# Performance work log

Hardware: AMD Instinct MI355X
Metric: run time of the kernel (lower is better)

## Reference

```python
import jax, jax.numpy as jnp
import numpy as np

PI = 3.1415  # the module hard-codes 3.1415, not math.pi


def setup_inputs() -> dict:
    nt, ns, nh, ng = 1000, 1024, 64, 32
    key = jax.random.key(0)
    kP, kE, kT1, kT2, kxc, kW, kb = jax.random.split(key, 7)
    # physically plausible forcings: P, E >= 0; T2 > T1 always
    P = jax.random.uniform(kP, (nt, ns)) * 10.0
    E = jax.random.uniform(kE, (nt, ns)) * 5.0
    T1 = jax.random.normal(kT1, (nt, ns)) * 10.0
    T2 = T1 + jax.random.uniform(kT2, (nt, ns)) * 10.0 + 0.1
    x = jnp.stack([P, E, T1, T2], axis=-1)  # [nt, ns, 4]
    xc = jax.random.normal(kxc, (ns, ng))
    std = 1.0 / np.sqrt(nh)  # reset_parameters: uniform(-std, std)
    W3 = jax.random.uniform(kW, (nh * 4, ng), minval=-std, maxval=std)
    b3 = jax.random.uniform(kb, (nh * 4,), minval=-std, maxval=std)
    return {"x": x, "xc": xc, "W3": W3, "b3": b3}


def reference(x, xc, W3, b3):
    nh = W3.shape[0] // 4
    P, E, T1, T2 = x[..., 0], x[..., 1], x[..., 2], x[..., 3]  # each [nt, ns]
    Ta = (T1 + T2) * 0.5
    melted = T1 >= 0.0
    frozen = T2 <= 0.0
    masked = melted | frozen
    # NaN-safe arccos: out-of-range args occur exactly where masked overrides apply
    arg = jnp.where(masked, 0.0, jnp.clip((T1 + T2) / (T2 - T1), -1.0, 1.0))
    rP = 1.0 - jnp.arccos(arg) / PI
    rP = jnp.where(melted, 1.0, jnp.where(frozen, 0.0, rP))
    Ps = (1.0 - rP) * P  # snow fraction
    Pl = rP * P          # liquid fraction
    # static gates (fc3 on catchment attributes); dropout is identity in eval
    w = xc @ W3.T + b3  # [ns, 4*nh]
    gm = jnp.exp(w[:, :nh]) + 1.0
    ge = jax.nn.sigmoid(w[:, nh:2 * nh])
    go = jax.nn.sigmoid(w[:, 2 * nh:3 * nh])
    ga = jax.nn.softmax(w[:, 3 * nh:], axis=1)

    ns = P.shape[1]
    S0 = jnp.zeros((ns, nh), dtype=x.dtype)
    H0 = jnp.zeros((ns, nh), dtype=x.dtype)

    def step(carry, inp):
        S0, H0 = carry
        Ps_k, Pl_k, E_k, Ta_k = inp  # each [ns]
        Sm = jnp.minimum(S0, jax.nn.relu(Ta_k[:, None] * gm))  # snowmelt
        S = S0 + Ps_k[:, None]
        H = jax.nn.relu(H0 + Sm + Pl_k[:, None] - E_k[:, None] * ge)
        Q = H * go
        Y = jnp.sum(Q * ga, axis=1)  # [ns]
        return (S - Sm, H - Q), Y

    _, Yout = jax.lax.scan(step, (S0, H0), (Ps, Pl, E, Ta))
    return Yout  # [nt, ns]
```

## Files before the change

kernel.cpp:

```cpp
#include <hip/hip_runtime.h>
#include <math.h>

#define NH 64
#define NG 32
#define LROW 68

__global__ __launch_bounds__(64) void waternet_kernel(
    const float* __restrict__ x,
    const float* __restrict__ xc,
    const float* __restrict__ W3,
    const float* __restrict__ b3,
    float* __restrict__ out,
    int nt, int ns)
{
    const int b    = blockIdx.x;
    const int s    = (b & 7) * (ns >> 3) + (b >> 3);
    const int lane = threadIdx.x;

    __shared__ float yb[2][NH * LROW];
    __shared__ float scal[NH * 4];

    float wq[4];
    #pragma unroll
    for (int q = 0; q < 4; ++q) {
        const float4* row = reinterpret_cast<const float4*>(W3 + (size_t)(q * NH + lane) * NG);
        const float4* xr  = reinterpret_cast<const float4*>(xc + (size_t)s * NG);
        float a = 0.f;
        #pragma unroll
        for (int g = 0; g < NG / 4; ++g) {
            const float4 w  = row[g];
            const float4 xv = xr[g];
            a = fmaf(w.x, xv.x, a); a = fmaf(w.y, xv.y, a);
            a = fmaf(w.z, xv.z, a); a = fmaf(w.w, xv.w, a);
        }
        wq[q] = a + b3[q * NH + lane];
    }
    const float gm = expf(wq[0]) + 1.0f;
    const float ge = 1.0f / (1.0f + expf(-wq[1]));
    const float go = 1.0f / (1.0f + expf(-wq[2]));
    float mx = wq[3];
    #pragma unroll
    for (int o = 32; o; o >>= 1) mx = fmaxf(mx, __shfl_xor(mx, o, 64));
    const float ex = expf(wq[3] - mx);
    float smx = ex;
    #pragma unroll
    for (int o = 32; o; o >>= 1) smx += __shfl_xor(smx, o, 64);
    const float ga = ex / smx;
    const float gq = go * ga;
    const float gk = 1.0f - go;

    float S = 0.f, H = 0.f;
    const int nfull = nt / NH;
    const int tail  = nt - nfull * NH;

    int tp = min(lane, nt - 1);
    float4 f = *reinterpret_cast<const float4*>(x + ((size_t)tp * ns + s) * 4);

    #define PHASE_A() { \
        const float P = f.x, E = f.y, T1 = f.z, T2 = f.w; \
        const float Ta  = 0.5f * (T1 + T2); \
        const float arg = fminf(1.f, fmaxf(-1.f, (T1 + T2) / (T2 - T1))); \
        const float aa  = fabsf(arg); \
        float p = fmaf(aa, -0.0012624911f, 0.0066700901f); \
        p = fmaf(aa, p, -0.0170881256f); p = fmaf(aa, p, 0.0308918810f); \
        p = fmaf(aa, p, -0.0501743046f); p = fmaf(aa, p, 0.0889789874f); \
        p = fmaf(aa, p, -0.2145988016f); p = fmaf(aa, p, 1.5707963050f); \
        const float rr0 = sqrtf(1.f - aa) * p;                   \
        const float ac  = (arg >= 0.f) ? rr0 : (3.14159265358979f - rr0); \
        const float rr  = 1.f - ac * (1.0f / 3.1415f);           \
        const float rP  = (T1 >= 0.f) ? 1.f : ((T2 <= 0.f) ? 0.f : rr); \
        float4 st; st.x = fmaxf(Ta, 0.f); st.y = (1.f - rP) * P; \
        st.z = rP * P;  st.w = E; \
        *reinterpret_cast<float4*>(&scal[lane * 4]) = st; \
    }

    #define STEP_BODY(sc, YB, J) { \
        const float M   = sc.x * gm;                      \
        const float Sm  = fminf(S, M);                    \
        const float tmp = fmaf(-sc.w, ge, sc.z);          \
        const float Hn  = fmaxf(H + Sm + tmp, 0.f); \
        S = (S + sc.y) - Sm; \
        H = Hn * gk; \
        (YB)[(J) * LROW + lane] = Hn * gq; \
    }

    for (int c = 0; c < nfull; ++c) {
        PHASE_A();

        tp = min((c + 1) * NH + lane, nt - 1);
        const float4 fn = *reinterpret_cast<const float4*>(x + ((size_t)tp * ns + s) * 4);

        float*       ybw = yb[c & 1];
        const float* ybr = yb[(c & 1) ^ 1];
        float z0 = 0.f, z1 = 0.f, z2 = 0.f, z3 = 0.f;

        #pragma unroll
        for (int j = 0; j < NH; ++j) {
            const float4 sc = *reinterpret_cast<const float4*>(&scal[j * 4]);
            STEP_BODY(sc, ybw, j)
            if ((j & 3) == 1) {
                const float4 v = *reinterpret_cast<const float4*>(&ybr[lane * LROW + (j >> 2) * 4]);
                z0 += v.x; z1 += v.y; z2 += v.z; z3 += v.w;
            }
        }
        if (c > 0)
            out[(size_t)((c - 1) * NH + lane) * ns + s] = (z0 + z1) + (z2 + z3);
        f = fn;
    }

    if (nfull > 0) {
        const float* row = &yb[(nfull - 1) & 1][lane * LROW];
        float z0 = 0.f, z1 = 0.f, z2 = 0.f, z3 = 0.f;
        #pragma unroll
        for (int g = 0; g < NH / 4; ++g) {
            const float4 v = *reinterpret_cast<const float4*>(&row[g * 4]);
            z0 += v.x; z1 += v.y; z2 += v.z; z3 += v.w;
        }
        out[(size_t)((nfull - 1) * NH + lane) * ns + s] = (z0 + z1) + (z2 + z3);
    }

    if (tail > 0) {
        PHASE_A();
        float* ybw = yb[nfull & 1];
        for (int j = 0; j < tail; ++j) {
            const float4 sc = *reinterpret_cast<const float4*>(&scal[j * 4]);
            STEP_BODY(sc, ybw, j)
        }
        if (lane < tail) {
            const float* row = &ybw[lane * LROW];
            float z0 = 0.f, z1 = 0.f, z2 = 0.f, z3 = 0.f;
            #pragma unroll
            for (int g = 0; g < NH / 4; ++g) {
                const float4 v = *reinterpret_cast<const float4*>(&row[g * 4]);
                z0 += v.x; z1 += v.y; z2 += v.z; z3 += v.w;
            }
            out[(size_t)(nfull * NH + lane) * ns + s] = (z0 + z1) + (z2 + z3);
        }
    }
    #undef PHASE_A
    #undef STEP_BODY
}

extern "C" void kernel_launch(void* const* d_in, const int* in_sizes, int n_in,
                              void* d_out, int out_size, void* d_ws, size_t ws_size,
                              hipStream_t stream) {
    const float* x  = (const float*)d_in[0];
    const float* xc = (const float*)d_in[1];
    const float* W3 = (const float*)d_in[2];
    const float* b3 = (const float*)d_in[3];
    float* out = (float*)d_out;

    const int nh = in_sizes[3] / 4;
    const int ng = in_sizes[2] / (4 * nh);
    const int ns = in_sizes[1] / ng;
    const int nt = in_sizes[0] / (ns * 4);

    waternet_kernel<<<dim3(ns), dim3(64), 0, stream>>>(x, xc, W3, b3, out, nt, ns);
}
```

Before: 111.6 us.

## Batch recurrence steps by eight and drop double-buffered reduction overlap

Restructures the per-chunk time loop into batches of eight steps that load the scalar forcings and precompute the independent melt thresholds and net inputs before the serial chain runs. The snow-melt min is rewritten as S - max(S-M, 0), which makes S = max(S-M,0) + Ps and shortens the dependent chain. The double-buffered output tile, which overlapped the previous chunk's reduction with the current recurrence, is replaced by a single tile reduced right after each chunk. This uses less shared memory but removes the reduction overlap, and the outer loop is kept from unrolling.

```diff
diff --git a/kernel.cpp b/kernel.cpp
--- a/kernel.cpp
+++ b/kernel.cpp
@@ -3,7 +3,7 @@
 
 #define NH 64
 #define NG 32
-#define LROW 68
+#define YROW 68
 
 __global__ __launch_bounds__(64) void waternet_kernel(
     const float* __restrict__ x,
@@ -17,7 +17,7 @@
     const int s    = (b & 7) * (ns >> 3) + (b >> 3);
     const int lane = threadIdx.x;
 
-    __shared__ float yb[2][NH * LROW];
+    __shared__ float ytile[NH * YROW];
     __shared__ float scal[NH * 4];
 
     float wq[4];
@@ -74,60 +74,66 @@
         *reinterpret_cast<float4*>(&scal[lane * 4]) = st; \
     }
 
-    #define STEP_BODY(sc, YB, J) { \
-        const float M   = sc.x * gm;                      \
-        const float Sm  = fminf(S, M);                    \
-        const float tmp = fmaf(-sc.w, ge, sc.z);          \
-        const float Hn  = fmaxf(H + Sm + tmp, 0.f); \
-        S = (S + sc.y) - Sm; \
-        H = Hn * gk; \
-        (YB)[(J) * LROW + lane] = Hn * gq; \
+    #define BATCH8(j0) { \
+        float4 sc[8]; float M[8], w[8]; \
+        _Pragma("unroll") \
+        for (int k = 0; k < 8; ++k) \
+            sc[k] = *reinterpret_cast<const float4*>(&scal[((j0) + k) * 4]);  \
+        _Pragma("unroll") \
+        for (int k = 0; k < 8; ++k) { M[k] = sc[k].x * gm; w[k] = fmaf(-sc[k].w, ge, sc[k].z); } \
+        _Pragma("unroll") \
+        for (int k = 0; k < 8; ++k) { \
+            const float u  = S - M[k]; \
+            const float um = fmaxf(u, 0.f);         \
+            const float Sm = S - um;                \
+            S = um + sc[k].y;                       \
+            const float a  = Sm + w[k]; \
+            const float Hn = fmaxf(H + a, 0.f); \
+            H = Hn * gk; \
+            ytile[((j0) + k) * YROW + lane] = Hn * gq; \
+        } \
     }
 
+    #pragma unroll 1
     for (int c = 0; c < nfull; ++c) {
         PHASE_A();
 
         tp = min((c + 1) * NH + lane, nt - 1);
         const float4 fn = *reinterpret_cast<const float4*>(x + ((size_t)tp * ns + s) * 4);
 
-        float*       ybw = yb[c & 1];
-        const float* ybr = yb[(c & 1) ^ 1];
-        float z0 = 0.f, z1 = 0.f, z2 = 0.f, z3 = 0.f;
+        #pragma unroll
+        for (int bb = 0; bb < NH / 8; ++bb) BATCH8(bb * 8)
 
-        #pragma unroll
-        for (int j = 0; j < NH; ++j) {
-            const float4 sc = *reinterpret_cast<const float4*>(&scal[j * 4]);
-            STEP_BODY(sc, ybw, j)
-            if ((j & 3) == 1) {
-                const float4 v = *reinterpret_cast<const float4*>(&ybr[lane * LROW + (j >> 2) * 4]);
+        {
+            const float* row = &ytile[lane * YROW];
+            float z0 = 0.f, z1 = 0.f, z2 = 0.f, z3 = 0.f;
+            #pragma unroll
+            for (int g = 0; g < NH / 4; ++g) {
+                const float4 v = *reinterpret_cast<const float4*>(&row[g * 4]);
                 z0 += v.x; z1 += v.y; z2 += v.z; z3 += v.w;
             }
+            out[(size_t)(c * NH + lane) * ns + s] = (z0 + z1) + (z2 + z3);
         }
-        if (c > 0)
-            out[(size_t)((c - 1) * NH + lane) * ns + s] = (z0 + z1) + (z2 + z3);
         f = fn;
-    }
-
-    if (nfull > 0) {
-        const float* row = &yb[(nfull - 1) & 1][lane * LROW];
-        float z0 = 0.f, z1 = 0.f, z2 = 0.f, z3 = 0.f;
-        #pragma unroll
-        for (int g = 0; g < NH / 4; ++g) {
-            const float4 v = *reinterpret_cast<const float4*>(&row[g * 4]);
-            z0 += v.x; z1 += v.y; z2 += v.z; z3 += v.w;
-        }
-        out[(size_t)((nfull - 1) * NH + lane) * ns + s] = (z0 + z1) + (z2 + z3);
     }
 
     if (tail > 0) {
         PHASE_A();
-        float* ybw = yb[nfull & 1];
-        for (int j = 0; j < tail; ++j) {
+        const int nb = tail / 8;
+        for (int bb = 0; bb < nb; ++bb) BATCH8(bb * 8)
+        for (int j = nb * 8; j < tail; ++j) {
             const float4 sc = *reinterpret_cast<const float4*>(&scal[j * 4]);
-            STEP_BODY(sc, ybw, j)
+            const float M  = sc.x * gm;
+            const float w  = fmaf(-sc.w, ge, sc.z);
+            const float um = fmaxf(S - M, 0.f);
+            const float Sm = S - um;
+            S = um + sc.y;
+            const float Hn = fmaxf(H + Sm + w, 0.f);
+            H = Hn * gk;
+            ytile[j * YROW + lane] = Hn * gq;
         }
         if (lane < tail) {
-            const float* row = &ybw[lane * LROW];
+            const float* row = &ytile[lane * YROW];
             float z0 = 0.f, z1 = 0.f, z2 = 0.f, z3 = 0.f;
             #pragma unroll
             for (int g = 0; g < NH / 4; ++g) {
@@ -138,7 +144,7 @@
         }
     }
     #undef PHASE_A
-    #undef STEP_BODY
+    #undef BATCH8
 }
 
 extern "C" void kernel_launch(void* const* d_in, const int* in_sizes, int n_in,
```

New measurement: 109.2 us. 2.1% less time.

## Split recurrence and forcing/reduction work across two warp-specialized wavefronts

Applied to the files above, without the earlier changes.

Blocks grow to two wavefronts. The first runs only the serial S/H recurrence, storing raw H per step. The second loads and preprocesses the next chunk's forcings and does the gq-weighted reduction of the previous chunk's H tile into the output. The intent is to take forcing loads, the arccos work and the output reduction off the critical recurrence path, and to lighten its step by folding the gq multiply into the reducer. In exchange it adds a __syncthreads per chunk, double-buffered scal, and more shared memory and threads per block.

```diff
diff --git a/kernel.cpp b/kernel.cpp
--- a/kernel.cpp
+++ b/kernel.cpp
@@ -3,9 +3,9 @@
 
 #define NH 64
 #define NG 32
-#define LROW 68
+#define YROW 68
 
-__global__ __launch_bounds__(64) void waternet_kernel(
+__global__ __launch_bounds__(128) void waternet_kernel(
     const float* __restrict__ x,
     const float* __restrict__ xc,
     const float* __restrict__ W3,
@@ -15,10 +15,13 @@
 {
     const int b    = blockIdx.x;
     const int s    = (b & 7) * (ns >> 3) + (b >> 3);
-    const int lane = threadIdx.x;
+    const int tid  = threadIdx.x;
+    const int lane = tid & 63;
+    const bool crit = (tid < 64);
 
-    __shared__ float yb[2][NH * LROW];
-    __shared__ float scal[NH * 4];
+    __shared__ float ytile[2][NH * YROW];
+    __shared__ float scal[2][NH * 4];
+    __shared__ float gqbuf[NH];
 
     float wq[4];
     #pragma unroll
@@ -49,15 +52,12 @@
     const float gq = go * ga;
     const float gk = 1.0f - go;
 
-    float S = 0.f, H = 0.f;
-    const int nfull = nt / NH;
-    const int tail  = nt - nfull * NH;
+    if (!crit) gqbuf[lane] = gq;
 
-    int tp = min(lane, nt - 1);
-    float4 f = *reinterpret_cast<const float4*>(x + ((size_t)tp * ns + s) * 4);
+    const int nchunk = (nt + NH - 1) / NH;
 
-    #define PHASE_A() { \
-        const float P = f.x, E = f.y, T1 = f.z, T2 = f.w; \
+    #define PHASE_A(f, dst) { \
+        const float P = (f).x, E = (f).y, T1 = (f).z, T2 = (f).w; \
         const float Ta  = 0.5f * (T1 + T2); \
         const float arg = fminf(1.f, fmaxf(-1.f, (T1 + T2) / (T2 - T1))); \
         const float aa  = fabsf(arg); \
@@ -65,80 +65,116 @@
         p = fmaf(aa, p, -0.0170881256f); p = fmaf(aa, p, 0.0308918810f); \
         p = fmaf(aa, p, -0.0501743046f); p = fmaf(aa, p, 0.0889789874f); \
         p = fmaf(aa, p, -0.2145988016f); p = fmaf(aa, p, 1.5707963050f); \
-        const float rr0 = sqrtf(1.f - aa) * p;                   \
+        const float rr0 = sqrtf(1.f - aa) * p; \
         const float ac  = (arg >= 0.f) ? rr0 : (3.14159265358979f - rr0); \
         const float rr  = 1.f - ac * (1.0f / 3.1415f);           \
         const float rP  = (T1 >= 0.f) ? 1.f : ((T2 <= 0.f) ? 0.f : rr); \
         float4 st; st.x = fmaxf(Ta, 0.f); st.y = (1.f - rP) * P; \
         st.z = rP * P;  st.w = E; \
-        *reinterpret_cast<float4*>(&scal[lane * 4]) = st; \
+        *reinterpret_cast<float4*>(&(dst)[lane * 4]) = st; \
     }
 
-    #define STEP_BODY(sc, YB, J) { \
-        const float M   = sc.x * gm;                      \
-        const float Sm  = fminf(S, M);                    \
-        const float tmp = fmaf(-sc.w, ge, sc.z);          \
-        const float Hn  = fmaxf(H + Sm + tmp, 0.f); \
-        S = (S + sc.y) - Sm; \
-        H = Hn * gk; \
-        (YB)[(J) * LROW + lane] = Hn * gq; \
+    #define LOAD8(dst, sp, j0) { \
+        _Pragma("unroll") \
+        for (int k = 0; k < 8; ++k) \
+            dst[k] = *reinterpret_cast<const float4*>(&(sp)[((j0) + k) * 4]); \
     }
 
-    for (int c = 0; c < nfull; ++c) {
-        PHASE_A();
-
-        tp = min((c + 1) * NH + lane, nt - 1);
-        const float4 fn = *reinterpret_cast<const float4*>(x + ((size_t)tp * ns + s) * 4);
-
-        float*       ybw = yb[c & 1];
-        const float* ybr = yb[(c & 1) ^ 1];
-        float z0 = 0.f, z1 = 0.f, z2 = 0.f, z3 = 0.f;
-
-        #pragma unroll
-        for (int j = 0; j < NH; ++j) {
-            const float4 sc = *reinterpret_cast<const float4*>(&scal[j * 4]);
-            STEP_BODY(sc, ybw, j)
-            if ((j & 3) == 1) {
-                const float4 v = *reinterpret_cast<const float4*>(&ybr[lane * LROW + (j >> 2) * 4]);
-                z0 += v.x; z1 += v.y; z2 += v.z; z3 += v.w;
-            }
-        }
-        if (c > 0)
-            out[(size_t)((c - 1) * NH + lane) * ns + s] = (z0 + z1) + (z2 + z3);
-        f = fn;
+    #define STEP(sc) { \
+        const float M  = (sc).x * gm; \
+        const float Sm = fminf(S, M); \
+        S = (S - Sm) + (sc).y; \
+        const float t2 = Sm + (sc).z; \
+        const float t3 = fmaf(-(sc).w, ge, t2); \
+        Hc = fmaxf(fmaf(gk, Hc, t3), 0.f); \
     }
 
-    if (nfull > 0) {
-        const float* row = &yb[(nfull - 1) & 1][lane * LROW];
+    if (!crit) {
+        const int tp = min(lane, nt - 1);
+        const float4 f = *reinterpret_cast<const float4*>(x + ((size_t)tp * ns + s) * 4);
+        PHASE_A(f, scal[0])
+    }
+    __syncthreads();
+
+    float S = 0.f, Hc = 0.f;
+
+    #pragma unroll 1
+    for (int c = 0; c < nchunk; ++c) {
+        const int cnt = min(NH, nt - c * NH);
+        if (crit) {
+            const float* sp = scal[c & 1];
+            float*       yb = &ytile[c & 1][lane * YROW];
+            if (cnt == NH) {
+                float4 sc[8], scn[8];
+                LOAD8(sc, sp, 0)
+                #pragma unroll
+                for (int bb = 0; bb < 8; ++bb) {
+                    if (bb < 7) LOAD8(scn, sp, (bb + 1) * 8)
+                    float yv[8];
+                    #pragma unroll
+                    for (int k = 0; k < 8; ++k) { STEP(sc[k]) yv[k] = Hc; }
+                    *reinterpret_cast<float4*>(yb + bb * 8)     = make_float4(yv[0], yv[1], yv[2], yv[3]);
+                    *reinterpret_cast<float4*>(yb + bb * 8 + 4) = make_float4(yv[4], yv[5], yv[6], yv[7]);
+                    if (bb < 7) {
+                        #pragma unroll
+                        for (int k = 0; k < 8; ++k) sc[k] = scn[k];
+                    }
+                }
+            } else {
+                const int nb = cnt / 8;
+                for (int bb = 0; bb < nb; ++bb) {
+                    float4 sc[8];
+                    LOAD8(sc, sp, bb * 8)
+                    float yv[8];
+                    #pragma unroll
+                    for (int k = 0; k < 8; ++k) { STEP(sc[k]) yv[k] = Hc; }
+                    *reinterpret_cast<float4*>(yb + bb * 8)     = make_float4(yv[0], yv[1], yv[2], yv[3]);
+                    *reinterpret_cast<float4*>(yb + bb * 8 + 4) = make_float4(yv[4], yv[5], yv[6], yv[7]);
+                }
+                for (int j = nb * 8; j < cnt; ++j) {
+                    const float4 sc = *reinterpret_cast<const float4*>(&sp[j * 4]);
+                    STEP(sc)
+                    yb[j] = Hc;
+                }
+            }
+        } else {
+            const int tp = min((c + 1) * NH + lane, nt - 1);
+            const float4 f = *reinterpret_cast<const float4*>(x + ((size_t)tp * ns + s) * 4);
+            if (c >= 1) {
+                const float* yr = ytile[(c - 1) & 1];
+                float z0 = 0.f, z1 = 0.f, z2 = 0.f, z3 = 0.f;
+                #pragma unroll
+                for (int h = 0; h < NH; h += 4) {
+                    z0 = fmaf(gqbuf[h + 0], yr[(h + 0) * YROW + lane], z0);
+                    z1 = fmaf(gqbuf[h + 1], yr[(h + 1) * YROW + lane], z1);
+                    z2 = fmaf(gqbuf[h + 2], yr[(h + 2) * YROW + lane], z2);
+                    z3 = fmaf(gqbuf[h + 3], yr[(h + 3) * YROW + lane], z3);
+                }
+                out[(size_t)((c - 1) * NH + lane) * ns + s] = (z0 + z1) + (z2 + z3);
+            }
+            PHASE_A(f, scal[(c + 1) & 1])
+        }
+        __syncthreads();
+    }
+
+    if (!crit) {
+        const int c   = nchunk - 1;
+        const int cnt = nt - c * NH;
+        const float* yr = ytile[c & 1];
         float z0 = 0.f, z1 = 0.f, z2 = 0.f, z3 = 0.f;
         #pragma unroll
-        for (int g = 0; g < NH / 4; ++g) {
-            const float4 v = *reinterpret_cast<const float4*>(&row[g * 4]);
-            z0 += v.x; z1 += v.y; z2 += v.z; z3 += v.w;
+        for (int h = 0; h < NH; h += 4) {
+            z0 = fmaf(gqbuf[h + 0], yr[(h + 0) * YROW + lane], z0);
+            z1 = fmaf(gqbuf[h + 1], yr[(h + 1) * YROW + lane], z1);
+            z2 = fmaf(gqbuf[h + 2], yr[(h + 2) * YROW + lane], z2);
+            z3 = fmaf(gqbuf[h + 3], yr[(h + 3) * YROW + lane], z3);
         }
-        out[(size_t)((nfull - 1) * NH + lane) * ns + s] = (z0 + z1) + (z2 + z3);
-    }
-
-    if (tail > 0) {
-        PHASE_A();
-        float* ybw = yb[nfull & 1];
-        for (int j = 0; j < tail; ++j) {
-            const float4 sc = *reinterpret_cast<const float4*>(&scal[j * 4]);
-            STEP_BODY(sc, ybw, j)
-        }
-        if (lane < tail) {
-            const float* row = &ybw[lane * LROW];
-            float z0 = 0.f, z1 = 0.f, z2 = 0.f, z3 = 0.f;
-            #pragma unroll
-            for (int g = 0; g < NH / 4; ++g) {
-                const float4 v = *reinterpret_cast<const float4*>(&row[g * 4]);
-                z0 += v.x; z1 += v.y; z2 += v.z; z3 += v.w;
-            }
-            out[(size_t)(nfull * NH + lane) * ns + s] = (z0 + z1) + (z2 + z3);
-        }
+        if (lane < cnt)
+            out[(size_t)(c * NH + lane) * ns + s] = (z0 + z1) + (z2 + z3);
     }
     #undef PHASE_A
-    #undef STEP_BODY
+    #undef LOAD8
+    #undef STEP
 }
 
 extern "C" void kernel_launch(void* const* d_in, const int* in_sizes, int n_in,
@@ -155,5 +191,5 @@
     const int ns = in_sizes[1] / ng;
     const int nt = in_sizes[0] / (ns * 4);
 
-    waternet_kernel<<<dim3(ns), dim3(64), 0, stream>>>(x, xc, W3, b3, out, nt, ns);
+    waternet_kernel<<<dim3(ns), dim3(128), 0, stream>>>(x, xc, W3, b3, out, nt, ns);
 }
```

Result: faster. 101.7 us (-8.9%).
